# Kernel tuning notes

Measured on AMD Instinct MI355X. Metric: run time of the kernel, lower is better.

## Reference

```python
import jax, jax.numpy as jnp
import numpy as np

B, T, D = 2, 2048, 2048
H, HK, HD = 16, 4, 128          # n_heads, n_kv_heads, head_dim
REP = H // HK                   # q heads per kv head
THETA = 10000.0


def _rope(x, cos, sin):
    # x: [B, T, h, HD]; cos/sin: [T, HD//2]
    # torch.view_as_complex pairs adjacent elements (x[...,2i], x[...,2i+1])
    xr, xi = x[..., ::2], x[..., 1::2]
    c = cos[None, :, None, :]
    s = sin[None, :, None, :]
    out_r = xr * c - xi * s
    out_i = xr * s + xi * c
    return jnp.stack([out_r, out_i], axis=-1).reshape(x.shape)


def setup_inputs() -> dict:
    key = jax.random.key(0)
    ks = jax.random.split(key, 5)
    x = jax.random.normal(ks[0], (B, T, D), dtype=jnp.float32)
    wq = jax.random.normal(ks[1], (D, H * HD), dtype=jnp.float32) * 0.02
    wk = jax.random.normal(ks[2], (D, HK * HD), dtype=jnp.float32) * 0.02
    wv = jax.random.normal(ks[3], (D, HK * HD), dtype=jnp.float32) * 0.02
    wo = jax.random.normal(ks[4], (H * HD, D), dtype=jnp.float32) * 0.02
    # rotary frequencies (precomputed freqs_cis, real/imag parts)
    inv_freq = 1.0 / (THETA ** (jnp.arange(0, HD, 2, dtype=jnp.float32) / HD))
    angles = jnp.arange(T, dtype=jnp.float32)[:, None] * inv_freq[None, :]  # [T, HD//2]
    freqs_cos = jnp.cos(angles)
    freqs_sin = jnp.sin(angles)
    # additive causal mask [T, T]
    mask = jnp.where(jnp.tril(jnp.ones((T, T), dtype=bool)), 0.0, -jnp.inf).astype(jnp.float32)
    return {"x": x, "freqs_cos": freqs_cos, "freqs_sin": freqs_sin, "mask": mask,
            "wq": wq, "wk": wk, "wv": wv, "wo": wo}


def reference(x, freqs_cos, freqs_sin, mask, wq, wk, wv, wo):
    q = (x @ wq).reshape(B, T, H, HD)
    k = (x @ wk).reshape(B, T, HK, HD)
    v = (x @ wv).reshape(B, T, HK, HD)
    q = _rope(q, freqs_cos, freqs_sin)
    k = _rope(k, freqs_cos, freqs_sin)
    scale = 1.0 / jnp.sqrt(jnp.float32(HD))
    # GQA: group q heads by kv head instead of expanding k/v
    qg = q.reshape(B, T, HK, REP, HD)
    attn = jnp.einsum('bqkrd,bskd->bkrqs', qg, k) * scale  # [B, HK, REP, T, T]
    attn = attn + mask[:T, :T]
    attn = jax.nn.softmax(attn, axis=-1)
    out = jnp.einsum('bkrqs,bskd->bqkrd', attn, v).reshape(B, T, H * HD)
    return out @ wo
```

## Files before the change

### kernel.cpp

```cpp
#include <hip/hip_runtime.h>
#include <hip/hip_bf16.h>


constexpr int BB  = 2;
constexpr int TT  = 2048;
constexpr int DD  = 2048;
constexpr int NHD = 16;
constexpr int NKV = 4;
constexpr int HDD = 128;
constexpr int MM  = BB * TT;
constexpr int KK  = DD;

typedef float  f32x4  __attribute__((ext_vector_type(4)));
typedef __bf16 bf16x8 __attribute__((ext_vector_type(8)));
typedef __bf16 bf16x4 __attribute__((ext_vector_type(4)));

__device__ __forceinline__ void async16(const void* g, void* l) {
  __builtin_amdgcn_global_load_lds(
      (const __attribute__((address_space(1))) unsigned int*)g,
      (__attribute__((address_space(3))) unsigned int*)l, 16, 0, 0);
}

__global__ __launch_bounds__(256) void k_cvt(const float* __restrict__ in,
                                             __bf16* __restrict__ out, int n) {
  int idx = (blockIdx.x * blockDim.x + threadIdx.x) * 4;
  int stride = gridDim.x * blockDim.x * 4;
  for (int i = idx; i < n; i += stride) {
    float4 v = *(const float4*)(in + i);
    bf16x4 o;
    o.x = (__bf16)v.x; o.y = (__bf16)v.y; o.z = (__bf16)v.z; o.w = (__bf16)v.w;
    *(bf16x4*)(out + i) = o;
  }
}

__global__ __launch_bounds__(256) void k_transpose_cvt(const float* __restrict__ in,
                                                       __bf16* __restrict__ out,
                                                       int K, int N) {
  __shared__ float tile[32][33];
  int n0 = blockIdx.x * 32, k0 = blockIdx.y * 32;
  int tx = threadIdx.x, ty = threadIdx.y;
#pragma unroll
  for (int i = 0; i < 4; ++i)
    tile[ty + i * 8][tx] = in[(size_t)(k0 + ty + i * 8) * N + n0 + tx];
  __syncthreads();
#pragma unroll
  for (int i = 0; i < 4; ++i)
    out[(size_t)(n0 + ty + i * 8) * K + k0 + tx] = (__bf16)tile[tx][ty + i * 8];
}

enum { EPI_QKV = 0, EPI_F32 = 1 };

template <int EPI>
__global__ __launch_bounds__(256, 2)
void k_gemm(const __bf16* __restrict__ A, const __bf16* __restrict__ BT,
            void* __restrict__ C0, void* __restrict__ C1, void* __restrict__ C2,
            const float* __restrict__ fcos, const float* __restrict__ fsin) {
  __shared__ __bf16 sA[128 * 64];
  __shared__ __bf16 sB[128 * 64];
  const int tid = threadIdx.x, wave = tid >> 6, lane = tid & 63;
  const int m0 = blockIdx.y * 128, n0 = blockIdx.x * 128;
  const int r = lane & 15, g = lane >> 4;
  const int wm = (wave >> 1) * 64, wn = (wave & 1) * 64;
  const int srow = lane >> 3;
  const int schunk = (lane & 7) ^ (srow & 7);

  f32x4 acc[4][4] = {};

  const __bf16* aBase = A + (size_t)m0 * KK + schunk * 8;
  const __bf16* bBase = BT + (size_t)n0 * KK + schunk * 8;

  for (int kt = 0; kt < KK; kt += 64) {
#pragma unroll
    for (int i = 0; i < 4; ++i) {
      int t = wave * 4 + i;
      int row = t * 8 + srow;
      async16(aBase + (size_t)row * KK + kt, (char*)sA + t * 1024);
      async16(bBase + (size_t)row * KK + kt, (char*)sB + t * 1024);
    }
    __syncthreads();
    bf16x8 af[4][2], bfr[4][2];
#pragma unroll
    for (int i = 0; i < 4; ++i) {
#pragma unroll
      for (int h = 0; h < 2; ++h) {
        int pc = (h * 4 + g) ^ (r & 7);
        af[i][h]  = *(const bf16x8*)((const char*)sA + (wm + i * 16 + r) * 128 + pc * 16);
        bfr[i][h] = *(const bf16x8*)((const char*)sB + (wn + i * 16 + r) * 128 + pc * 16);
      }
    }
#pragma unroll
    for (int i = 0; i < 4; ++i)
#pragma unroll
      for (int j = 0; j < 4; ++j) {
        acc[i][j] = __builtin_amdgcn_mfma_f32_16x16x32_bf16(af[i][0], bfr[j][0], acc[i][j], 0, 0, 0);
        acc[i][j] = __builtin_amdgcn_mfma_f32_16x16x32_bf16(af[i][1], bfr[j][1], acc[i][j], 0, 0, 0);
      }
    __syncthreads();
  }

#pragma unroll
  for (int i = 0; i < 4; ++i) {
#pragma unroll
    for (int j = 0; j < 4; ++j) {
#pragma unroll
      for (int jj = 0; jj < 4; ++jj) {
        int rm = m0 + wm + i * 16 + g * 4 + jj;
        int cn = n0 + wn + j * 16 + r;
        float v = acc[i][j][jj];
        if constexpr (EPI == EPI_F32) {
          ((float*)C0)[(size_t)rm * 2048 + cn] = v;
        } else {
          int b = rm >> 11, t = rm & (TT - 1);
          if (cn < 2048) {
            int hh = cn >> 7, hd = cn & 127;
            float pv = __shfl_xor(v, 1);
            float c = fcos[t * 64 + (hd >> 1)], s = fsin[t * 64 + (hd >> 1)];
            float ov = (hd & 1) ? (pv * s + v * c) : (v * c - pv * s);
            ((__bf16*)C0)[((size_t)(b * NHD + hh) * TT + t) * HDD + hd] = (__bf16)ov;
          } else if (cn < 2560) {
            int c2 = cn - 2048, hh = c2 >> 7, hd = c2 & 127;
            float pv = __shfl_xor(v, 1);
            float c = fcos[t * 64 + (hd >> 1)], s = fsin[t * 64 + (hd >> 1)];
            float ov = (hd & 1) ? (pv * s + v * c) : (v * c - pv * s);
            ((__bf16*)C1)[((size_t)(b * NKV + hh) * TT + t) * HDD + hd] = (__bf16)ov;
          } else {
            int c2 = cn - 2560, hh = c2 >> 7, hd = c2 & 127;
            ((__bf16*)C2)[((size_t)(b * NKV + hh) * HDD + hd) * TT + t] = (__bf16)v;
          }
        }
      }
    }
  }
}

__device__ __forceinline__ void attn_tile(
    const bf16x8 qf[4], f32x4 o[8], float* mrun, float* lrun,
    const __bf16* sKb, const __bf16* sVb, __bf16* sPw,
    bool diag, int qrow0, int kv0, int r, int g) {
  f32x4 sa[4] = {};
#pragma unroll
  for (int nf = 0; nf < 4; ++nf)
#pragma unroll
    for (int kh = 0; kh < 4; ++kh) {
      int row = nf * 16 + r;
      int pc = (kh * 4 + g) ^ (row & 15);
      bf16x8 kf = *(const bf16x8*)((const char*)sKb + row * 256 + pc * 16);
      sa[nf] = __builtin_amdgcn_mfma_f32_16x16x32_bf16(qf[kh], kf, sa[nf], 0, 0, 0);
    }
  const float SC = 0.08838834764831845f;
#pragma unroll
  for (int nf = 0; nf < 4; ++nf)
#pragma unroll
    for (int jj = 0; jj < 4; ++jj) {
      float s = sa[nf][jj] * SC;
      if (diag && (kv0 + nf * 16 + r > qrow0 + g * 4 + jj)) s = -1e30f;
      sa[nf][jj] = s;
    }
  float mnew[4], scf[4], tsum[4];
#pragma unroll
  for (int jj = 0; jj < 4; ++jj) {
    float mx = fmaxf(fmaxf(sa[0][jj], sa[1][jj]), fmaxf(sa[2][jj], sa[3][jj]));
    mx = fmaxf(mx, __shfl_xor(mx, 1));
    mx = fmaxf(mx, __shfl_xor(mx, 2));
    mx = fmaxf(mx, __shfl_xor(mx, 4));
    mx = fmaxf(mx, __shfl_xor(mx, 8));
    mnew[jj] = fmaxf(mrun[jj], mx);
    scf[jj] = __expf(mrun[jj] - mnew[jj]);
    mrun[jj] = mnew[jj];
    tsum[jj] = 0.f;
  }
#pragma unroll
  for (int nf = 0; nf < 4; ++nf)
#pragma unroll
    for (int jj = 0; jj < 4; ++jj) {
      float p = __expf(sa[nf][jj] - mnew[jj]);
      tsum[jj] += p;
      int row = g * 4 + jj;
      int col = nf * 16 + r;
      int pcw = (col >> 3) ^ (row & 7);
      *((__bf16*)((char*)sPw + row * 128 + pcw * 16 + (col & 7) * 2)) = (__bf16)p;
    }
#pragma unroll
  for (int jj = 0; jj < 4; ++jj) {
    float ts = tsum[jj];
    ts += __shfl_xor(ts, 1);
    ts += __shfl_xor(ts, 2);
    ts += __shfl_xor(ts, 4);
    ts += __shfl_xor(ts, 8);
    lrun[jj] = lrun[jj] * scf[jj] + ts;
#pragma unroll
    for (int nf = 0; nf < 8; ++nf) o[nf][jj] *= scf[jj];
  }
  bf16x8 pf[2];
#pragma unroll
  for (int k2 = 0; k2 < 2; ++k2) {
    int pc = (k2 * 4 + g) ^ (r & 7);
    pf[k2] = *(const bf16x8*)((const char*)sPw + r * 128 + pc * 16);
  }
#pragma unroll
  for (int nf = 0; nf < 8; ++nf)
#pragma unroll
    for (int k2 = 0; k2 < 2; ++k2) {
      int row = nf * 16 + r;
      int pc = (k2 * 4 + g) ^ (row & 7);
      bf16x8 vf = *(const bf16x8*)((const char*)sVb + row * 128 + pc * 16);
      o[nf] = __builtin_amdgcn_mfma_f32_16x16x32_bf16(pf[k2], vf, o[nf], 0, 0, 0);
    }
}

__global__ __launch_bounds__(256, 2)
void k_attn(const __bf16* __restrict__ Q, const __bf16* __restrict__ Kc,
            const __bf16* __restrict__ VT, __bf16* __restrict__ Out) {
  __shared__ __bf16 sK[2][64 * 128];
  __shared__ __bf16 sV[2][128 * 64];
  __shared__ __bf16 sP[4][16 * 64];

  const int tid = threadIdx.x, wave = tid >> 6, lane = tid & 63;
  const int pa = blockIdx.x;
  const int h = blockIdx.y, b = blockIdx.z;
  const int kvh = h >> 2;
  const int r = lane & 15, g = lane >> 4;

  const __bf16* Qp = Q + ((size_t)(b * NHD + h) * TT) * HDD;
  const __bf16* Kp = Kc + ((size_t)(b * NKV + kvh) * TT) * HDD;
  const __bf16* Vp = VT + ((size_t)(b * NKV + kvh) * HDD) * TT;

  auto stage = [&](int kv0, int buf) {
#pragma unroll
    for (int i = 0; i < 4; ++i) {
      int ti = wave * 4 + i;
      int rowk = ti * 4 + (lane >> 4);
      int sck = (lane & 15) ^ (rowk & 15);
      async16(Kp + (size_t)(kv0 + rowk) * HDD + sck * 8, (char*)sK[buf] + ti * 1024);
      int rowv = ti * 8 + (lane >> 3);
      int scv = (lane & 7) ^ (rowv & 7);
      async16(Vp + (size_t)rowv * TT + kv0 + scv * 8, (char*)sV[buf] + ti * 1024);
    }
  };

  auto run_qtile = [&](int qt) {
    const int q00 = qt * 64;
    bf16x8 qf[4];
#pragma unroll
    for (int kh = 0; kh < 4; ++kh)
      qf[kh] = *(const bf16x8*)(Qp + (size_t)(q00 + wave * 16 + r) * HDD + kh * 32 + g * 8);
    f32x4 o[8] = {};
    float m[4], l[4];
#pragma unroll
    for (int jj = 0; jj < 4; ++jj) { m[jj] = -1e30f; l[jj] = 0.f; }

    __syncthreads();
    stage(0, 0);
    for (int it = 0; it <= qt; ++it) {
      __syncthreads();
      if (it < qt) stage((it + 1) * 64, (it + 1) & 1);
      attn_tile(qf, o, m, l, sK[it & 1], sV[it & 1], sP[wave],
                it == qt, q00 + wave * 16, it * 64, r, g);
    }
#pragma unroll
    for (int jj = 0; jj < 4; ++jj) {
      float inv = 1.f / l[jj];
      int t = q00 + wave * 16 + g * 4 + jj;
#pragma unroll
      for (int nf = 0; nf < 8; ++nf) {
        int hd = nf * 16 + r;
        Out[((size_t)(b * TT + t)) * 2048 + h * 128 + hd] = (__bf16)(o[nf][jj] * inv);
      }
    }
  };

  run_qtile(31 - pa);
  run_qtile(pa);
}

constexpr size_t OFF_XB   = 0;
constexpr size_t OFF_WQKV = OFF_XB + (size_t)MM * KK * 2;
constexpr size_t OFF_WOT  = OFF_WQKV + (size_t)3072 * KK * 2;
constexpr size_t OFF_QB   = OFF_WOT + (size_t)2048 * KK * 2;
constexpr size_t OFF_KB   = OFF_QB + (size_t)MM * 2048 * 2;
constexpr size_t OFF_VTB  = OFF_KB + (size_t)BB * NKV * TT * HDD * 2;
constexpr size_t OFF_ATT  = OFF_VTB + (size_t)BB * NKV * TT * HDD * 2;

extern "C" void kernel_launch(void* const* d_in, const int* in_sizes, int n_in,
                              void* d_out, int out_size, void* d_ws, size_t ws_size,
                              hipStream_t stream) {
  const float* x    = (const float*)d_in[0];
  const float* fcos = (const float*)d_in[1];
  const float* fsin = (const float*)d_in[2];
  const float* wq = (const float*)d_in[4];
  const float* wk = (const float*)d_in[5];
  const float* wv = (const float*)d_in[6];
  const float* wo = (const float*)d_in[7];
  float* out = (float*)d_out;
  char* ws = (char*)d_ws;

  __bf16* xb    = (__bf16*)(ws + OFF_XB);
  __bf16* wqkvT = (__bf16*)(ws + OFF_WQKV);
  __bf16* woT   = (__bf16*)(ws + OFF_WOT);
  __bf16* Qb    = (__bf16*)(ws + OFF_QB);
  __bf16* Kb    = (__bf16*)(ws + OFF_KB);
  __bf16* VTb   = (__bf16*)(ws + OFF_VTB);
  __bf16* attb  = (__bf16*)(ws + OFF_ATT);

  k_cvt<<<1024, 256, 0, stream>>>(x, xb, MM * KK);
  dim3 tb(32, 8);
  k_transpose_cvt<<<dim3(2048 / 32, KK / 32), tb, 0, stream>>>(wq, wqkvT, KK, 2048);
  k_transpose_cvt<<<dim3(512 / 32, KK / 32), tb, 0, stream>>>(wk, wqkvT + (size_t)2048 * KK, KK, 512);
  k_transpose_cvt<<<dim3(512 / 32, KK / 32), tb, 0, stream>>>(wv, wqkvT + (size_t)2560 * KK, KK, 512);
  k_transpose_cvt<<<dim3(2048 / 32, KK / 32), tb, 0, stream>>>(wo, woT, KK, 2048);

  k_gemm<EPI_QKV><<<dim3(3072 / 128, MM / 128), 256, 0, stream>>>(
      xb, wqkvT, Qb, Kb, VTb, fcos, fsin);

  k_attn<<<dim3(16, NHD, BB), 256, 0, stream>>>(Qb, Kb, VTb, attb);

  k_gemm<EPI_F32><<<dim3(2048 / 128, MM / 128), 256, 0, stream>>>(
      attb, woT, out, nullptr, nullptr, nullptr, nullptr);
}
```

Measured before the change: 330.9 us.

## Fuse QKV weight transposes, add coalesced V transpose, lazy softmax rescale

Result: no change. 332.7 us (+0.5%).

```diff
diff --git a/kernel.cpp b/kernel.cpp
--- a/kernel.cpp
+++ b/kernel.cpp
@@ -48,10 +48,49 @@
     out[(size_t)(n0 + ty + i * 8) * K + k0 + tx] = (__bf16)tile[tx][ty + i * 8];
 }
 
+__global__ __launch_bounds__(256) void k_transpose_qkv(const float* __restrict__ wq,
+                                                       const float* __restrict__ wk,
+                                                       const float* __restrict__ wv,
+                                                       __bf16* __restrict__ out) {
+  __shared__ float tile[32][33];
+  int n0 = blockIdx.x * 32, k0 = blockIdx.y * 32;
+  int tx = threadIdx.x, ty = threadIdx.y;
+  const float* src; int nn, srcN;
+  if (n0 < 2048)      { src = wq; nn = n0;        srcN = 2048; }
+  else if (n0 < 2560) { src = wk; nn = n0 - 2048; srcN = 512; }
+  else                { src = wv; nn = n0 - 2560; srcN = 512; }
+#pragma unroll
+  for (int i = 0; i < 4; ++i)
+    tile[ty + i * 8][tx] = src[(size_t)(k0 + ty + i * 8) * srcN + nn + tx];
+  __syncthreads();
+#pragma unroll
+  for (int i = 0; i < 4; ++i)
+    out[(size_t)(n0 + ty + i * 8) * KK + k0 + tx] = (__bf16)tile[tx][ty + i * 8];
+}
+
+__global__ __launch_bounds__(256) void k_vtrans(const __bf16* __restrict__ in,
+                                                __bf16* __restrict__ out) {
+  __shared__ __bf16 tile[32][33];
+  int c0 = blockIdx.x * 32;
+  int t0 = blockIdx.y * 32;
+  int b  = blockIdx.z;
+  int tx = threadIdx.x, ty = threadIdx.y;
+#pragma unroll
+  for (int i = 0; i < 4; ++i)
+    tile[ty + i * 8][tx] = in[((size_t)b * TT + t0 + ty + i * 8) * 512 + c0 + tx];
+  __syncthreads();
+#pragma unroll
+  for (int i = 0; i < 4; ++i) {
+    int c = c0 + ty + i * 8;
+    out[(((size_t)b * NKV + (c >> 7)) * HDD + (c & 127)) * TT + t0 + tx] =
+        tile[tx][ty + i * 8];
+  }
+}
+
 enum { EPI_QKV = 0, EPI_F32 = 1 };
 
 template <int EPI>
-__global__ __launch_bounds__(256, 2)
+__global__ __launch_bounds__(256, 3)
 void k_gemm(const __bf16* __restrict__ A, const __bf16* __restrict__ BT,
             void* __restrict__ C0, void* __restrict__ C1, void* __restrict__ C2,
             const float* __restrict__ fcos, const float* __restrict__ fsin) {
@@ -124,8 +163,8 @@
             float ov = (hd & 1) ? (pv * s + v * c) : (v * c - pv * s);
             ((__bf16*)C1)[((size_t)(b * NKV + hh) * TT + t) * HDD + hd] = (__bf16)ov;
           } else {
-            int c2 = cn - 2560, hh = c2 >> 7, hd = c2 & 127;
-            ((__bf16*)C2)[((size_t)(b * NKV + hh) * HDD + hd) * TT + t] = (__bf16)v;
+            int c2 = cn - 2560;
+            ((__bf16*)C2)[(size_t)rm * 512 + c2] = (__bf16)v;
           }
         }
       }
@@ -148,15 +187,14 @@
       sa[nf] = __builtin_amdgcn_mfma_f32_16x16x32_bf16(qf[kh], kf, sa[nf], 0, 0, 0);
     }
   const float SC = 0.08838834764831845f;
-#pragma unroll
-  for (int nf = 0; nf < 4; ++nf)
-#pragma unroll
-    for (int jj = 0; jj < 4; ++jj) {
-      float s = sa[nf][jj] * SC;
-      if (diag && (kv0 + nf * 16 + r > qrow0 + g * 4 + jj)) s = -1e30f;
-      sa[nf][jj] = s;
-    }
-  float mnew[4], scf[4], tsum[4];
+  if (diag) {
+#pragma unroll
+    for (int nf = 0; nf < 4; ++nf)
+#pragma unroll
+      for (int jj = 0; jj < 4; ++jj)
+        if (kv0 + nf * 16 + r > qrow0 + g * 4 + jj) sa[nf][jj] = -1e30f;
+  }
+  float pmax[4];
 #pragma unroll
   for (int jj = 0; jj < 4; ++jj) {
     float mx = fmaxf(fmaxf(sa[0][jj], sa[1][jj]), fmaxf(sa[2][jj], sa[3][jj]));
@@ -164,16 +202,28 @@
     mx = fmaxf(mx, __shfl_xor(mx, 2));
     mx = fmaxf(mx, __shfl_xor(mx, 4));
     mx = fmaxf(mx, __shfl_xor(mx, 8));
-    mnew[jj] = fmaxf(mrun[jj], mx);
-    scf[jj] = __expf(mrun[jj] - mnew[jj]);
-    mrun[jj] = mnew[jj];
-    tsum[jj] = 0.f;
-  }
+    pmax[jj] = mx;
+  }
+  const float THR = 8.0f / SC;
+  float gmax = fmaxf(fmaxf(pmax[0] - mrun[0], pmax[1] - mrun[1]),
+                     fmaxf(pmax[2] - mrun[2], pmax[3] - mrun[3]));
+  if (!__all(gmax <= THR)) {
+#pragma unroll
+    for (int jj = 0; jj < 4; ++jj) {
+      float mnew = fmaxf(mrun[jj], pmax[jj]);
+      float scf = __expf(SC * (mrun[jj] - mnew));
+      mrun[jj] = mnew;
+      lrun[jj] *= scf;
+#pragma unroll
+      for (int nf = 0; nf < 8; ++nf) o[nf][jj] *= scf;
+    }
+  }
+  float tsum[4] = {0.f, 0.f, 0.f, 0.f};
 #pragma unroll
   for (int nf = 0; nf < 4; ++nf)
 #pragma unroll
     for (int jj = 0; jj < 4; ++jj) {
-      float p = __expf(sa[nf][jj] - mnew[jj]);
+      float p = __expf(SC * (sa[nf][jj] - mrun[jj]));
       tsum[jj] += p;
       int row = g * 4 + jj;
       int col = nf * 16 + r;
@@ -187,9 +237,7 @@
     ts += __shfl_xor(ts, 2);
     ts += __shfl_xor(ts, 4);
     ts += __shfl_xor(ts, 8);
-    lrun[jj] = lrun[jj] * scf[jj] + ts;
-#pragma unroll
-    for (int nf = 0; nf < 8; ++nf) o[nf][jj] *= scf[jj];
+    lrun[jj] += ts;
   }
   bf16x8 pf[2];
 #pragma unroll
@@ -278,7 +326,8 @@
 constexpr size_t OFF_WOT  = OFF_WQKV + (size_t)3072 * KK * 2;
 constexpr size_t OFF_QB   = OFF_WOT + (size_t)2048 * KK * 2;
 constexpr size_t OFF_KB   = OFF_QB + (size_t)MM * 2048 * 2;
-constexpr size_t OFF_VTB  = OFF_KB + (size_t)BB * NKV * TT * HDD * 2;
+constexpr size_t OFF_VB   = OFF_KB + (size_t)BB * NKV * TT * HDD * 2;
+constexpr size_t OFF_VTB  = OFF_VB + (size_t)MM * 512 * 2;
 constexpr size_t OFF_ATT  = OFF_VTB + (size_t)BB * NKV * TT * HDD * 2;
 
 extern "C" void kernel_launch(void* const* d_in, const int* in_sizes, int n_in,
@@ -299,18 +348,19 @@
   __bf16* woT   = (__bf16*)(ws + OFF_WOT);
   __bf16* Qb    = (__bf16*)(ws + OFF_QB);
   __bf16* Kb    = (__bf16*)(ws + OFF_KB);
+  __bf16* Vb    = (__bf16*)(ws + OFF_VB);
   __bf16* VTb   = (__bf16*)(ws + OFF_VTB);
   __bf16* attb  = (__bf16*)(ws + OFF_ATT);
 
   k_cvt<<<1024, 256, 0, stream>>>(x, xb, MM * KK);
   dim3 tb(32, 8);
-  k_transpose_cvt<<<dim3(2048 / 32, KK / 32), tb, 0, stream>>>(wq, wqkvT, KK, 2048);
-  k_transpose_cvt<<<dim3(512 / 32, KK / 32), tb, 0, stream>>>(wk, wqkvT + (size_t)2048 * KK, KK, 512);
-  k_transpose_cvt<<<dim3(512 / 32, KK / 32), tb, 0, stream>>>(wv, wqkvT + (size_t)2560 * KK, KK, 512);
+  k_transpose_qkv<<<dim3(3072 / 32, KK / 32), tb, 0, stream>>>(wq, wk, wv, wqkvT);
   k_transpose_cvt<<<dim3(2048 / 32, KK / 32), tb, 0, stream>>>(wo, woT, KK, 2048);
 
   k_gemm<EPI_QKV><<<dim3(3072 / 128, MM / 128), 256, 0, stream>>>(
-      xb, wqkvT, Qb, Kb, VTb, fcos, fsin);
+      xb, wqkvT, Qb, Kb, Vb, fcos, fsin);
+
+  k_vtrans<<<dim3(512 / 32, TT / 32, BB), tb, 0, stream>>>(Vb, VTb);
 
   k_attn<<<dim3(16, NHD, BB), 256, 0, stream>>>(Qb, Kb, VTb, attb);
 
```
